# Optimization experiments

Hardware: AMD Instinct MI355X
Metric: run time of the kernel (lower is better)

Reference implementation:

```python
import jax, jax.numpy as jnp
import numpy as np


def setup_inputs() -> dict:
    key = jax.random.key(0)
    k1, k2, k3 = jax.random.split(key, 3)
    B, D, C = 16384, 1024, 14
    z_image = jax.random.normal(k1, (B, D), dtype=jnp.float32)
    z_text = jax.random.normal(k2, (B, D), dtype=jnp.float32)
    labels = jax.random.randint(k3, (B, C), 0, 2, dtype=jnp.int32)
    return {"z_image": z_image, "z_text": z_text, "labels": labels}


def _margins(labels):
    # labels: [B, C] binary; imposter index j = (i+1) % B -> roll by -1
    lj = jnp.roll(labels, -1, axis=0)
    equal = jnp.all(labels == lj, axis=1)                     # [B]
    n = jnp.sum(labels | lj, axis=1).astype(jnp.float32)      # union size
    d = jnp.sum(labels ^ lj, axis=1).astype(jnp.float32)      # hamming diff
    m = jnp.where(n > 0, jnp.maximum(0.5, d / jnp.maximum(n, 1.0)), 0.5)
    return jnp.where(equal, 0.0, m)                           # [B]


def reference(z_image, z_text, labels):
    # similarity_function == 'dot' (default path of the torch module)
    margin = _margins(labels)                                  # [B]
    paired = jnp.sum(z_image * z_text, axis=1)                 # dot(img_i, txt_i)
    imp_img = jnp.sum(jnp.roll(z_image, -1, axis=0) * z_text, axis=1)  # dot(img_j, txt_i)
    imp_txt = jnp.sum(jnp.roll(z_text, -1, axis=0) * z_image, axis=1)  # dot(txt_j, img_i)
    loss_img = jnp.mean(jax.nn.relu(imp_img - paired + margin))
    loss_txt = jnp.mean(jax.nn.relu(imp_txt - paired + margin))
    return loss_img + loss_txt
```

## Files before the change

kernel.cpp:

```cpp
#include <hip/hip_runtime.h>


constexpr int D   = 1024;
constexpr int C   = 14;
constexpr int RPW = 4;
constexpr int WPB = 4;
constexpr int RPB = RPW * WPB;

__device__ __forceinline__ float dot4(const float4 x, const float4 y) {
    return x.x * y.x + x.y * y.y + x.z * y.z + x.w * y.w;
}

__global__ __launch_bounds__(256) void rank_phase1(
    const float* __restrict__ zi, const float* __restrict__ zt,
    const int* __restrict__ labels, float* __restrict__ partial, int B)
{
    const int wave = threadIdx.x >> 6;
    const int lane = threadIdx.x & 63;
    const int r0   = blockIdx.x * RPB + wave * RPW;
    const int M    = B - 1;

    const float4* zi_r[RPW + 1];
    const float4* zt_r[RPW + 1];
    #pragma unroll
    for (int k = 0; k <= RPW; ++k) {
        const int r = (r0 + k) & M;
        zi_r[k] = (const float4*)(zi + (size_t)r * D);
        zt_r[k] = (const float4*)(zt + (size_t)r * D);
    }

    float p [RPW] = {0.f, 0.f, 0.f, 0.f};
    float ii[RPW] = {0.f, 0.f, 0.f, 0.f};
    float it[RPW] = {0.f, 0.f, 0.f, 0.f};

    #pragma unroll
    for (int j = 0; j < 4; ++j) {
        const int idx = lane + 64 * j;
        float4 a[RPW + 1], b[RPW + 1];
        #pragma unroll
        for (int k = 0; k <= RPW; ++k) a[k] = zi_r[k][idx];
        #pragma unroll
        for (int k = 0; k <= RPW; ++k) b[k] = zt_r[k][idx];
        #pragma unroll
        for (int k = 0; k < RPW; ++k) {
            p [k] += dot4(a[k],     b[k]);
            ii[k] += dot4(a[k + 1], b[k]);
            it[k] += dot4(b[k + 1], a[k]);
        }
    }

    const int kk = lane >> 4;
    const int c  = lane & 15;
    int lx = 0, lo = 0;
    if (c < C) {
        const int ra = (r0 + kk)     & M;
        const int rb = (r0 + kk + 1) & M;
        const int li = labels[(size_t)ra * C + c];
        const int lj = labels[(size_t)rb * C + c];
        lx = li ^ lj;
        lo = li | lj;
    }
    const unsigned long long bx = __ballot(lx != 0);
    const unsigned long long bo = __ballot(lo != 0);

    #pragma unroll
    for (int off = 32; off > 0; off >>= 1) {
        #pragma unroll
        for (int k = 0; k < RPW; ++k) {
            p [k] += __shfl_down(p [k], off, 64);
            ii[k] += __shfl_down(ii[k], off, 64);
            it[k] += __shfl_down(it[k], off, 64);
        }
    }

    float local = 0.f;
    if (lane == 0) {
        #pragma unroll
        for (int k = 0; k < RPW; ++k) {
            const float dv = (float)__popcll((bx >> (16 * k)) & 0x3FFFull);
            const float nv = (float)__popcll((bo >> (16 * k)) & 0x3FFFull);
            const float m  = (dv == 0.f) ? 0.f : fmaxf(0.5f, dv / nv);
            local += fmaxf(ii[k] - p[k] + m, 0.f)
                   + fmaxf(it[k] - p[k] + m, 0.f);
        }
    }

    __shared__ float smem[WPB];
    if (lane == 0) smem[wave] = local;
    __syncthreads();
    if (threadIdx.x == 0)
        partial[blockIdx.x] = smem[0] + smem[1] + smem[2] + smem[3];
}

__global__ __launch_bounds__(256) void rank_phase2(
    const float* __restrict__ partial, float* __restrict__ out,
    int npart, float invB)
{
    float s = 0.f;
    for (int i = threadIdx.x; i < npart; i += 256) s += partial[i];
    #pragma unroll
    for (int off = 32; off > 0; off >>= 1) s += __shfl_down(s, off, 64);
    __shared__ float sm[4];
    if ((threadIdx.x & 63) == 0) sm[threadIdx.x >> 6] = s;
    __syncthreads();
    if (threadIdx.x == 0)
        out[0] = (sm[0] + sm[1] + sm[2] + sm[3]) * invB;
}

extern "C" void kernel_launch(void* const* d_in, const int* in_sizes, int n_in,
                              void* d_out, int out_size, void* d_ws, size_t ws_size,
                              hipStream_t stream) {
    const float* zi     = (const float*)d_in[0];
    const float* zt     = (const float*)d_in[1];
    const int*   labels = (const int*)d_in[2];
    float*       out    = (float*)d_out;
    float*       ws     = (float*)d_ws;

    const int B      = in_sizes[0] / D;
    const int blocks = B / RPB;

    rank_phase1<<<blocks, 256, 0, stream>>>(zi, zt, labels, ws, B);
    rank_phase2<<<1, 256, 0, stream>>>(ws, out, blocks, 1.0f / (float)B);
}
```

Measured before the change: 150.0 us.

## Split feature dimension across waves and reduce row dots via shared memory

Each block now handles 4 rows, with the four waves splitting the 1024-wide feature dimension rather than each wave owning 4 rows. Per-wave partial dot products are combined in shared memory before thread 0 computes the hinge terms. This quadruples the block count and issues all loads up front to raise memory-level parallelism. It adds a shared-memory cross-wave reduction and more blocks and partials for the second phase.

Result: no change. 151.2 us (+0.8%).

```diff
diff --git a/kernel.cpp b/kernel.cpp
--- a/kernel.cpp
+++ b/kernel.cpp
@@ -3,9 +3,8 @@
 
 constexpr int D   = 1024;
 constexpr int C   = 14;
-constexpr int RPW = 4;
+constexpr int RPB = 4;
 constexpr int WPB = 4;
-constexpr int RPB = RPW * WPB;
 
 __device__ __forceinline__ float dot4(const float4 x, const float4 y) {
     return x.x * y.x + x.y * y.y + x.z * y.z + x.w * y.w;
@@ -17,79 +16,82 @@
 {
     const int wave = threadIdx.x >> 6;
     const int lane = threadIdx.x & 63;
-    const int r0   = blockIdx.x * RPB + wave * RPW;
+    const int r0   = blockIdx.x * RPB;
     const int M    = B - 1;
+    const int idx  = wave * 64 + lane;
 
-    const float4* zi_r[RPW + 1];
-    const float4* zt_r[RPW + 1];
+    float4 a[RPB + 1], b[RPB + 1];
     #pragma unroll
-    for (int k = 0; k <= RPW; ++k) {
+    for (int k = 0; k <= RPB; ++k) {
         const int r = (r0 + k) & M;
-        zi_r[k] = (const float4*)(zi + (size_t)r * D);
-        zt_r[k] = (const float4*)(zt + (size_t)r * D);
+        a[k] = ((const float4*)(zi + (size_t)r * D))[idx];
+        b[k] = ((const float4*)(zt + (size_t)r * D))[idx];
     }
 
-    float p [RPW] = {0.f, 0.f, 0.f, 0.f};
-    float ii[RPW] = {0.f, 0.f, 0.f, 0.f};
-    float it[RPW] = {0.f, 0.f, 0.f, 0.f};
-
+    float p[RPB], ii[RPB], it[RPB];
     #pragma unroll
-    for (int j = 0; j < 4; ++j) {
-        const int idx = lane + 64 * j;
-        float4 a[RPW + 1], b[RPW + 1];
-        #pragma unroll
-        for (int k = 0; k <= RPW; ++k) a[k] = zi_r[k][idx];
-        #pragma unroll
-        for (int k = 0; k <= RPW; ++k) b[k] = zt_r[k][idx];
-        #pragma unroll
-        for (int k = 0; k < RPW; ++k) {
-            p [k] += dot4(a[k],     b[k]);
-            ii[k] += dot4(a[k + 1], b[k]);
-            it[k] += dot4(b[k + 1], a[k]);
-        }
+    for (int k = 0; k < RPB; ++k) {
+        p [k] = dot4(a[k],     b[k]);
+        ii[k] = dot4(a[k + 1], b[k]);
+        it[k] = dot4(b[k + 1], a[k]);
     }
 
-    const int kk = lane >> 4;
-    const int c  = lane & 15;
-    int lx = 0, lo = 0;
-    if (c < C) {
-        const int ra = (r0 + kk)     & M;
-        const int rb = (r0 + kk + 1) & M;
-        const int li = labels[(size_t)ra * C + c];
-        const int lj = labels[(size_t)rb * C + c];
-        lx = li ^ lj;
-        lo = li | lj;
+    unsigned long long bx = 0, bo = 0;
+    if (wave == 0) {
+        const int kk = lane >> 4;
+        const int c  = lane & 15;
+        int lx = 0, lo = 0;
+        if (c < C) {
+            const int ra = (r0 + kk)     & M;
+            const int rb = (r0 + kk + 1) & M;
+            const int li = labels[(size_t)ra * C + c];
+            const int lj = labels[(size_t)rb * C + c];
+            lx = li ^ lj;
+            lo = li | lj;
+        }
+        bx = __ballot(lx != 0);
+        bo = __ballot(lo != 0);
     }
-    const unsigned long long bx = __ballot(lx != 0);
-    const unsigned long long bo = __ballot(lo != 0);
 
     #pragma unroll
     for (int off = 32; off > 0; off >>= 1) {
         #pragma unroll
-        for (int k = 0; k < RPW; ++k) {
+        for (int k = 0; k < RPB; ++k) {
             p [k] += __shfl_down(p [k], off, 64);
             ii[k] += __shfl_down(ii[k], off, 64);
             it[k] += __shfl_down(it[k], off, 64);
         }
     }
 
-    float local = 0.f;
+    __shared__ float sm[WPB][12];
     if (lane == 0) {
         #pragma unroll
-        for (int k = 0; k < RPW; ++k) {
+        for (int k = 0; k < RPB; ++k) {
+            sm[wave][k * 3 + 0] = p [k];
+            sm[wave][k * 3 + 1] = ii[k];
+            sm[wave][k * 3 + 2] = it[k];
+        }
+    }
+    __syncthreads();
+
+    if (threadIdx.x == 0) {
+        float local = 0.f;
+        #pragma unroll
+        for (int k = 0; k < RPB; ++k) {
+            float ps = 0.f, is = 0.f, ts = 0.f;
+            #pragma unroll
+            for (int w = 0; w < WPB; ++w) {
+                ps += sm[w][k * 3 + 0];
+                is += sm[w][k * 3 + 1];
+                ts += sm[w][k * 3 + 2];
+            }
             const float dv = (float)__popcll((bx >> (16 * k)) & 0x3FFFull);
             const float nv = (float)__popcll((bo >> (16 * k)) & 0x3FFFull);
             const float m  = (dv == 0.f) ? 0.f : fmaxf(0.5f, dv / nv);
-            local += fmaxf(ii[k] - p[k] + m, 0.f)
-                   + fmaxf(it[k] - p[k] + m, 0.f);
+            local += fmaxf(is - ps + m, 0.f) + fmaxf(ts - ps + m, 0.f);
         }
+        partial[blockIdx.x] = local;
     }
-
-    __shared__ float smem[WPB];
-    if (lane == 0) smem[wave] = local;
-    __syncthreads();
-    if (threadIdx.x == 0)
-        partial[blockIdx.x] = smem[0] + smem[1] + smem[2] + smem[3];
 }
 
 __global__ __launch_bounds__(256) void rank_phase2(
```

## Assign one row per 16-thread group instead of four rows per wave

Applied to the files above, without the earlier changes.

Each row is now handled by a 16-thread group that also loads the next row's image and text vectors directly. Before, a wave handled four consecutive rows and shared the neighbour-row loads among them. Each group reduces with xor-shuffles over 16 lanes, and one lane computes the label margin with int2 loads. The change raises parallelism and shortens the reductions, but it drops in-wave reuse of the neighbour rows, so each row is read twice from global memory (cache may absorb some of this). Launch bounds now request 2 blocks per CU.

Result: slower. 155.7 us (+3.8%).

```diff
diff --git a/kernel.cpp b/kernel.cpp
--- a/kernel.cpp
+++ b/kernel.cpp
@@ -1,95 +1,78 @@
 #include <hip/hip_runtime.h>
 
 
-constexpr int D   = 1024;
-constexpr int C   = 14;
-constexpr int RPW = 4;
-constexpr int WPB = 4;
-constexpr int RPB = RPW * WPB;
+constexpr int D      = 1024;
+constexpr int C      = 14;
+constexpr int TPR    = 16;
+constexpr int RPB    = 256 / TPR;
+constexpr int CHUNKS = D / 4 / TPR;
 
 __device__ __forceinline__ float dot4(const float4 x, const float4 y) {
     return x.x * y.x + x.y * y.y + x.z * y.z + x.w * y.w;
 }
 
-__global__ __launch_bounds__(256) void rank_phase1(
+__global__ __launch_bounds__(256, 2) void rank_phase1(
     const float* __restrict__ zi, const float* __restrict__ zt,
     const int* __restrict__ labels, float* __restrict__ partial, int B)
 {
-    const int wave = threadIdx.x >> 6;
-    const int lane = threadIdx.x & 63;
-    const int r0   = blockIdx.x * RPB + wave * RPW;
+    const int t    = threadIdx.x;
+    const int rsub = t >> 4;
+    const int csub = t & 15;
+    const int row  = blockIdx.x * RPB + rsub;
     const int M    = B - 1;
+    const int nrow = (row + 1) & M;
 
-    const float4* zi_r[RPW + 1];
-    const float4* zt_r[RPW + 1];
-    #pragma unroll
-    for (int k = 0; k <= RPW; ++k) {
-        const int r = (r0 + k) & M;
-        zi_r[k] = (const float4*)(zi + (size_t)r * D);
-        zt_r[k] = (const float4*)(zt + (size_t)r * D);
+    float margin = 0.f;
+    if (csub == 0) {
+        const int2* La = (const int2*)(labels + (size_t)row  * C);
+        const int2* Lb = (const int2*)(labels + (size_t)nrow * C);
+        int dv = 0, nv = 0;
+        #pragma unroll
+        for (int q = 0; q < C / 2; ++q) {
+            const int2 x = La[q];
+            const int2 y = Lb[q];
+            dv += (x.x ^ y.x) + (x.y ^ y.y);
+            nv += (x.x | y.x) + (x.y | y.y);
+        }
+        margin = (dv == 0) ? 0.f : fmaxf(0.5f, (float)dv / (float)nv);
     }
 
-    float p [RPW] = {0.f, 0.f, 0.f, 0.f};
-    float ii[RPW] = {0.f, 0.f, 0.f, 0.f};
-    float it[RPW] = {0.f, 0.f, 0.f, 0.f};
+    const float4* Ar  = (const float4*)(zi + (size_t)row  * D);
+    const float4* Br  = (const float4*)(zt + (size_t)row  * D);
+    const float4* Ar1 = (const float4*)(zi + (size_t)nrow * D);
+    const float4* Br1 = (const float4*)(zt + (size_t)nrow * D);
+
+    float p = 0.f, ii = 0.f, it = 0.f;
+    #pragma unroll
+    for (int c = 0; c < CHUNKS; ++c) {
+        const int idx = csub + TPR * c;
+        const float4 a  = Ar [idx];
+        const float4 b  = Br [idx];
+        const float4 a1 = Ar1[idx];
+        const float4 b1 = Br1[idx];
+        p  += dot4(a,  b);
+        ii += dot4(a1, b);
+        it += dot4(b1, a);
+    }
 
     #pragma unroll
-    for (int j = 0; j < 4; ++j) {
-        const int idx = lane + 64 * j;
-        float4 a[RPW + 1], b[RPW + 1];
-        #pragma unroll
-        for (int k = 0; k <= RPW; ++k) a[k] = zi_r[k][idx];
-        #pragma unroll
-        for (int k = 0; k <= RPW; ++k) b[k] = zt_r[k][idx];
-        #pragma unroll
-        for (int k = 0; k < RPW; ++k) {
-            p [k] += dot4(a[k],     b[k]);
-            ii[k] += dot4(a[k + 1], b[k]);
-            it[k] += dot4(b[k + 1], a[k]);
-        }
+    for (int off = 1; off < TPR; off <<= 1) {
+        p  += __shfl_xor(p,  off, 64);
+        ii += __shfl_xor(ii, off, 64);
+        it += __shfl_xor(it, off, 64);
     }
 
-    const int kk = lane >> 4;
-    const int c  = lane & 15;
-    int lx = 0, lo = 0;
-    if (c < C) {
-        const int ra = (r0 + kk)     & M;
-        const int rb = (r0 + kk + 1) & M;
-        const int li = labels[(size_t)ra * C + c];
-        const int lj = labels[(size_t)rb * C + c];
-        lx = li ^ lj;
-        lo = li | lj;
+    __shared__ float sm[RPB];
+    if (csub == 0)
+        sm[rsub] = fmaxf(ii - p + margin, 0.f)
+                 + fmaxf(it - p + margin, 0.f);
+    __syncthreads();
+    if (t == 0) {
+        float s = 0.f;
+        #pragma unroll
+        for (int k = 0; k < RPB; ++k) s += sm[k];
+        partial[blockIdx.x] = s;
     }
-    const unsigned long long bx = __ballot(lx != 0);
-    const unsigned long long bo = __ballot(lo != 0);
-
-    #pragma unroll
-    for (int off = 32; off > 0; off >>= 1) {
-        #pragma unroll
-        for (int k = 0; k < RPW; ++k) {
-            p [k] += __shfl_down(p [k], off, 64);
-            ii[k] += __shfl_down(ii[k], off, 64);
-            it[k] += __shfl_down(it[k], off, 64);
-        }
-    }
-
-    float local = 0.f;
-    if (lane == 0) {
-        #pragma unroll
-        for (int k = 0; k < RPW; ++k) {
-            const float dv = (float)__popcll((bx >> (16 * k)) & 0x3FFFull);
-            const float nv = (float)__popcll((bo >> (16 * k)) & 0x3FFFull);
-            const float m  = (dv == 0.f) ? 0.f : fmaxf(0.5f, dv / nv);
-            local += fmaxf(ii[k] - p[k] + m, 0.f)
-                   + fmaxf(it[k] - p[k] + m, 0.f);
-        }
-    }
-
-    __shared__ float smem[WPB];
-    if (lane == 0) smem[wave] = local;
-    __syncthreads();
-    if (threadIdx.x == 0)
-        partial[blockIdx.x] = smem[0] + smem[1] + smem[2] + smem[3];
 }
 
 __global__ __launch_bounds__(256) void rank_phase2(
```
